# Optimization experiments

Hardware: AMD Instinct MI355X
Metric: run time of the kernel (lower is better)

## Reference

```python
import jax, jax.numpy as jnp
import numpy as np

B = 128      # graphs per batch
NPG = 40     # nodes per graph (<= MAXN)
N = B * NPG  # total nodes
E = 20000    # total edges
LP = 512     # protein sequence length
NPROT = 229  # KIBA proteins
MAXN = 45    # to_dense_batch max_num_nodes


def _gcn(x, W, b, src, dst, n):
    # PyG GCNConv: symmetric-normalized adjacency with self-loops.
    xw = x @ W
    deg = jnp.zeros((n,), xw.dtype).at[dst].add(1.0) + 1.0  # +1 for self-loop
    dinv = jax.lax.rsqrt(deg)
    msg = xw[src] * (dinv[src] * dinv[dst])[:, None]
    agg = jnp.zeros_like(xw).at[dst].add(msg) + xw * (1.0 / deg)[:, None]
    return agg + b


def _to_dense_batch(x, batch, num_graphs, max_nodes):
    n = x.shape[0]
    counts = jnp.zeros((num_graphs,), jnp.int32).at[batch].add(1)
    starts = jnp.concatenate([jnp.zeros((1,), jnp.int32), jnp.cumsum(counts)[:-1].astype(jnp.int32)])
    pos = jnp.arange(n, dtype=jnp.int32) - starts[batch]
    idx = batch * max_nodes + pos
    dense = jnp.zeros((num_graphs * max_nodes, x.shape[1]), x.dtype).at[idx].set(x)
    return dense.reshape(num_graphs, max_nodes, x.shape[1])


def setup_inputs() -> dict:
    key = jax.random.key(0)
    ks = jax.random.split(key, 32)
    xav = lambda k, s: jax.random.normal(k, s, jnp.float32) * jnp.sqrt(2.0 / (s[0] + s[-1]))
    x = jax.random.normal(ks[0], (N, 78), jnp.float32)
    src = jax.random.randint(ks[1], (E,), 0, N)
    dst = (src // NPG) * NPG + jax.random.randint(ks[2], (E,), 0, NPG)  # intra-graph edges
    edge_index = jnp.stack([src, dst]).astype(jnp.int32)
    target_id = jax.random.randint(ks[3], (B,), 0, NPROT).astype(jnp.int32)
    batch = (jnp.arange(N) // NPG).astype(jnp.int32)
    proteins = jax.random.normal(ks[4], (NPROT, LP, 1280), jnp.float32) * 0.1
    return dict(
        x=x, edge_index=edge_index, target_id=target_id, batch=batch, proteins=proteins,
        gW1=xav(ks[5], (78, 128)), gb1=jnp.zeros((128,), jnp.float32),
        gW2=xav(ks[6], (128, 128)), gb2=jnp.zeros((128,), jnp.float32),
        gW3=xav(ks[7], (128, 256)), gb3=jnp.zeros((256,), jnp.float32),
        fc1_W=xav(ks[8], (256, 1024)), fc1_b=jnp.zeros((1024,), jnp.float32),
        fc2_W=xav(ks[9], (1024, 128)), fc2_b=jnp.zeros((128,), jnp.float32),
        bert1_W=xav(ks[10], (1280, 128)), bert1_b=jnp.zeros((128,), jnp.float32),
        bert2_W=xav(ks[11], (128, 128)), bert2_b=jnp.zeros((128,), jnp.float32),
        W_b=xav(ks[12], (128, 128)), W_c=xav(ks[13], (32, 128)), W_p=xav(ks[14], (32, 128)),
        w_hc=xav(ks[15], (32, 1)), w_hp=xav(ks[16], (32, 1)),
        cat1_W=xav(ks[17], (256, 1024)), cat1_b=jnp.zeros((1024,), jnp.float32),
        cat2_W=xav(ks[18], (1024, 512)), cat2_b=jnp.zeros((512,), jnp.float32),
        out_W=xav(ks[19], (512, 1)), out_b=jnp.zeros((1,), jnp.float32),
    )


def _forward(x, proteins, gW1, gb1, gW2, gb2, gW3, gb3, fc1_W, fc1_b, fc2_W, fc2_b,
             bert1_W, bert1_b, bert2_W, bert2_b, W_b, W_c, W_p, w_hc, w_hp,
             cat1_W, cat1_b, cat2_W, cat2_b, out_W, out_b,
             edge_index, target_id, batch):
    relu, tanh = jax.nn.relu, jnp.tanh
    src, dst = edge_index[0], edge_index[1]
    # --- GCN stack (dropout is identity in eval) ---
    h = relu(_gcn(x, gW1, gb1, src, dst, x.shape[0]))
    h = relu(_gcn(h, gW2, gb2, src, dst, x.shape[0]))
    h = relu(_gcn(h, gW3, gb3, src, dst, x.shape[0]))  # [N, 256]
    hd = _to_dense_batch(h, batch, B, MAXN)            # [B, 45, 256]
    hd = relu(hd @ fc1_W + fc1_b)
    hd = relu(hd @ fc2_W + fc2_b)                      # [B, 45, 128]
    xc = jnp.transpose(hd, (0, 2, 1))                  # [B, 128, 45]
    # --- protein branch ---
    t = proteins[target_id]                            # [B, LP, 1280]
    t = relu(t @ bert1_W + bert1_b)
    t = relu(t @ bert2_W + bert2_b)                    # [B, LP, 128]
    # --- parallel co-attention ---
    C = tanh(jnp.einsum('blk,km,bms->bls', t, W_b, xc))       # [B, LP, 45]
    Wcx = jnp.einsum('km,bms->bks', W_c, xc)                  # [B, 32, 45]
    Wpt = jnp.einsum('km,blm->bkl', W_p, t)                   # [B, 32, LP]
    H_c = tanh(Wcx + jnp.einsum('bkl,bls->bks', Wpt, C))      # [B, 32, 45]
    H_p = tanh(Wpt + jnp.einsum('bks,bls->bkl', Wcx, C))      # [B, 32, LP]
    a_c = jax.nn.softmax(jnp.einsum('k,bks->bs', w_hc[:, 0], H_c), axis=-1)  # [B, 45]
    a_p = jax.nn.softmax(jnp.einsum('k,bkl->bl', w_hp[:, 0], H_p), axis=-1)  # [B, LP]
    c = jnp.einsum('bs,bms->bm', a_c, xc)                     # [B, 128]
    p = jnp.einsum('bl,blm->bm', a_p, t)                      # [B, 128]
    cp = jnp.concatenate([c, p], axis=1)                      # [B, 256]
    cp = relu(cp @ cat1_W + cat1_b)
    cp = relu(cp @ cat2_W + cat2_b)
    return cp @ out_W + out_b                                 # [B, 1]


def reference(x, edge_index, target_id, batch, proteins, gW1, gb1, gW2, gb2, gW3, gb3,
              fc1_W, fc1_b, fc2_W, fc2_b, bert1_W, bert1_b, bert2_W, bert2_b,
              W_b, W_c, W_p, w_hc, w_hp, cat1_W, cat1_b, cat2_W, cat2_b, out_W, out_b):
    return _forward(x, proteins, gW1, gb1, gW2, gb2, gW3, gb3, fc1_W, fc1_b, fc2_W, fc2_b,
                    bert1_W, bert1_b, bert2_W, bert2_b, W_b, W_c, W_p, w_hc, w_hp,
                    cat1_W, cat1_b, cat2_W, cat2_b, out_W, out_b,
                    edge_index, target_id, batch)
```

## Files before the change

### kernel.cpp

```cpp
#include <hip/hip_runtime.h>
#include <hip/hip_bf16.h>

typedef __hip_bfloat16 bf16;
typedef __bf16 bf16x8 __attribute__((ext_vector_type(8)));
typedef float f32x4 __attribute__((ext_vector_type(4)));

#define NB   128
#define NPGX 40
#define NNODE 5120
#define NE   20000
#define LPX  512
#define MAXNX 45

__device__ __forceinline__ void stv(float* p, float v) { *p = v; }
__device__ __forceinline__ void stv(bf16* p, float v) { *p = __float2bfloat16(v); }
__device__ __forceinline__ ushort f2bf(float f) {
    uint x = __float_as_uint(f);
    return (ushort)((x + 0x7fffu + ((x >> 16) & 1u)) >> 16);
}
__device__ __forceinline__ float bf2f(ushort u) { return __uint_as_float(((uint)u) << 16); }
__device__ __forceinline__ float dot4(f32x4 a, f32x4 b) {
    return a[0]*b[0] + a[1]*b[1] + a[2]*b[2] + a[3]*b[3];
}

template <typename TA, typename TO, int ACT, bool GATHER>
__global__ __launch_bounds__(256) void gemm_mfma(
    const TA* __restrict__ A, const ushort* __restrict__ BT, const float* __restrict__ bias,
    TO* __restrict__ C, int M, int N, int K, const int* __restrict__ tgt)
{
    __shared__ __align__(16) ushort sA[128][40];
    __shared__ __align__(16) ushort sB[128][40];
    const int t = threadIdx.x;
    const int lane = t & 63;
    const int wave = t >> 6;
    const int wr = wave >> 1, wc = wave & 1;
    const int m0 = blockIdx.x * 128;
    const int n0 = blockIdx.y * 128;
    const int fr = lane & 15;
    const int kh = lane >> 4;

    f32x4 acc[4][4] = {};

    for (int k0 = 0; k0 < K; k0 += 32) {
        if constexpr (sizeof(TA) == 2) {
            const ushort* Ap = (const ushort*)A;
#pragma unroll
            for (int i = 0; i < 2; i++) {
                int linear = i * 2048 + t * 8;
                int row = linear >> 5, k = linear & 31;
                long gr = m0 + row;
                uint4 v = *(const uint4*)(Ap + gr * (long)K + k0 + k);
                *(uint4*)&sA[row][k] = v;
            }
        } else {
            const float* Ap = (const float*)A;
#pragma unroll
            for (int i = 0; i < 4; i++) {
                int linear = i * 1024 + t * 4;
                int row = linear >> 5, k = linear & 31;
                long gr = m0 + row;
                if (GATHER) { int bb = (int)(gr >> 9); gr = (long)tgt[bb] * LPX + (gr & 511); }
                float4 v = *(const float4*)(Ap + gr * (long)K + k0 + k);
                ushort4 h;
                h.x = f2bf(v.x); h.y = f2bf(v.y); h.z = f2bf(v.z); h.w = f2bf(v.w);
                *(ushort4*)&sA[row][k] = h;
            }
        }
#pragma unroll
        for (int i = 0; i < 2; i++) {
            int linear = i * 2048 + t * 8;
            int row = linear >> 5, k = linear & 31;
            uint4 v = *(const uint4*)(BT + (long)(n0 + row) * K + k0 + k);
            *(uint4*)&sB[row][k] = v;
        }
        __syncthreads();

        bf16x8 a[4], b[4];
#pragma unroll
        for (int mf = 0; mf < 4; mf++)
            a[mf] = *(const bf16x8*)&sA[wr * 64 + mf * 16 + fr][kh * 8];
#pragma unroll
        for (int nf = 0; nf < 4; nf++)
            b[nf] = *(const bf16x8*)&sB[wc * 64 + nf * 16 + fr][kh * 8];
#pragma unroll
        for (int mf = 0; mf < 4; mf++)
#pragma unroll
            for (int nf = 0; nf < 4; nf++)
                acc[mf][nf] = __builtin_amdgcn_mfma_f32_16x16x32_bf16(a[mf], b[nf], acc[mf][nf], 0, 0, 0);
        __syncthreads();
    }

#pragma unroll
    for (int mf = 0; mf < 4; mf++) {
#pragma unroll
        for (int nf = 0; nf < 4; nf++) {
            int coln = n0 + wc * 64 + nf * 16 + fr;
            float bv = bias ? bias[coln] : 0.f;
#pragma unroll
            for (int r = 0; r < 4; r++) {
                int row = m0 + wr * 64 + mf * 16 + kh * 4 + r;
                float v = acc[mf][nf][r] + bv;
                if (ACT == 1) v = fmaxf(v, 0.f);
                else if (ACT == 2) v = tanhf(v);
                stv(&C[(long)row * N + coln], v);
            }
        }
    }
}

__global__ __launch_bounds__(256) void k_transp_all(
    const float* __restrict__ s0, const float* __restrict__ s1, const float* __restrict__ s2,
    const float* __restrict__ s3,
    ushort* __restrict__ d0, ushort* __restrict__ d1, ushort* __restrict__ d2,
    ushort* __restrict__ d3)
{
    __shared__ float s[32][33];
    int bid = blockIdx.x;
    const float* in; ushort* out; int K, N, b;
    if (bid < 256)      { in = s0; out = d0; K = 256;  N = 1024; b = bid; }
    else if (bid < 384) { in = s1; out = d1; K = 1024; N = 128;  b = bid - 256; }
    else if (bid < 544) { in = s2; out = d2; K = 1280; N = 128;  b = bid - 384; }
    else                { in = s3; out = d3; K = 128;  N = 128;  b = bid - 544; }
    int ktiles = K / 32;
    int kt = (b % ktiles) * 32, nt = (b / ktiles) * 32;
    int t = threadIdx.x;
    int tn = t & 31, tk = t >> 5;
#pragma unroll
    for (int i = 0; i < 4; i++)
        s[tk + i * 8][tn] = in[(long)(kt + tk + i * 8) * N + nt + tn];
    __syncthreads();
#pragma unroll
    for (int i = 0; i < 4; i++)
        out[(long)(nt + tk + i * 8) * K + kt + tn] = f2bf(s[tn][tk + i * 8]);
}

__global__ void k_count(const int* __restrict__ dst, int* __restrict__ cnt, int E) {
    int e = blockIdx.x * 256 + threadIdx.x;
    if (e < E) atomicAdd(&cnt[dst[e]], 1);
}

__global__ void k_scan(const int* __restrict__ cnt, int* __restrict__ row_start,
                       float* __restrict__ dinv, float* __restrict__ deginv, int n) {
    __shared__ int sd[1024];
    __shared__ int scarry;
    int t = threadIdx.x;
    if (t == 0) scarry = 0;
    __syncthreads();
    for (int base = 0; base < n; base += 1024) {
        int i = base + t;
        int v = (i < n) ? cnt[i] : 0;
        sd[t] = v;
        __syncthreads();
        for (int off = 1; off < 1024; off <<= 1) {
            int tmp = (t >= off) ? sd[t - off] : 0;
            __syncthreads();
            sd[t] += tmp;
            __syncthreads();
        }
        int carry = scarry;
        if (i < n) {
            row_start[i] = carry + sd[t] - v;
            float deg = (float)(v + 1);
            dinv[i] = rsqrtf(deg);
            deginv[i] = 1.f / deg;
        }
        __syncthreads();
        if (t == 1023) scarry = carry + sd[1023];
        __syncthreads();
    }
    if (t == 0) row_start[n] = scarry;
}

__global__ void k_fill(const int* __restrict__ src, const int* __restrict__ dst,
                       const int* __restrict__ row_start, int* __restrict__ cursor,
                       int* __restrict__ col, float* __restrict__ val,
                       const float* __restrict__ dinv, int E) {
    int e = blockIdx.x * 256 + threadIdx.x;
    if (e >= E) return;
    int d = dst[e], s = src[e];
    int p = atomicAdd(&cursor[d], 1);
    int idx = row_start[d] + p;
    col[idx] = s;
    val[idx] = dinv[s] * dinv[d];
}

__device__ __forceinline__ void gcn_gemm(const float (*hin)[132], float (*hout)[260],
                                         float (*sW)[260], const float* __restrict__ Wg,
                                         int K, int N, int NQ, int t) {
    f32x4 acc[10] = {};
    for (int k0 = 0; k0 < K; k0 += 32) {
        int kmax = min(32, K - k0);
        int kpad = (kmax + 3) & ~3;
        __syncthreads();
        for (int o = t; o < kpad * N; o += 256) {
            int row = o / N, c = o - row * N;
            sW[row][c] = (row < kmax) ? Wg[(k0 + row) * N + c] : 0.f;
        }
        __syncthreads();
        for (int kk = 0; kk < kpad; kk += 4) {
#pragma unroll 10
            for (int j = 0; j < NQ; j++) {
                int q = t + j * 256;
                int i = q / (N / 4), f = (q % (N / 4)) * 4;
                f32x4 hv = *(const f32x4*)&hin[i][k0 + kk];
#pragma unroll
                for (int d = 0; d < 4; d++) {
                    f32x4 wv = *(const f32x4*)&sW[kk + d][f];
                    acc[j][0] = fmaf(hv[d], wv[0], acc[j][0]);
                    acc[j][1] = fmaf(hv[d], wv[1], acc[j][1]);
                    acc[j][2] = fmaf(hv[d], wv[2], acc[j][2]);
                    acc[j][3] = fmaf(hv[d], wv[3], acc[j][3]);
                }
            }
        }
    }
    __syncthreads();
#pragma unroll 10
    for (int j = 0; j < NQ; j++) {
        int q = t + j * 256;
        int i = q / (N / 4), f = (q % (N / 4)) * 4;
        *(f32x4*)&hout[i][f] = acc[j];
    }
}

__device__ __forceinline__ void gcn_agg(const float (*hout)[260], float (*hin)[132],
                                        const float* __restrict__ bias,
                                        const float* __restrict__ deginv,
                                        const int* __restrict__ row_start,
                                        const int* __restrict__ col,
                                        const float* __restrict__ val,
                                        float* __restrict__ hd, int N, bool tohd, int g, int t) {
    int base = g * NPGX;
    for (int o = t; o < 40 * N; o += 256) {
        int i = o / N, f = o - i * N;
        float s = hout[i][f] * deginv[base + i];
        int e0 = row_start[base + i], e1 = row_start[base + i + 1];
        for (int e = e0; e < e1; e++) s += val[e] * hout[col[e] - base][f];
        s += bias[f];
        s = fmaxf(s, 0.f);
        if (tohd) hd[(g * MAXNX + i) * N + f] = s;
        else      hin[i][f] = s;
    }
    if (tohd) for (int o = t; o < 5 * N; o += 256) hd[(g * MAXNX + 40) * N + o] = 0.f;
}

__global__ __launch_bounds__(256) void k_gcn(
    const float* __restrict__ x,
    const float* __restrict__ W1, const float* __restrict__ b1,
    const float* __restrict__ W2, const float* __restrict__ b2,
    const float* __restrict__ W3, const float* __restrict__ b3,
    const float* __restrict__ deginv, const int* __restrict__ row_start,
    const int* __restrict__ col, const float* __restrict__ val,
    float* __restrict__ hd)
{
    int g = blockIdx.x, t = threadIdx.x;
    __shared__ __align__(16) float hin[40][132];
    __shared__ __align__(16) float hout[40][260];
    __shared__ __align__(16) float sW[32][260];
    for (int o = t; o < 40 * 78; o += 256) hin[o / 78][o % 78] = x[(g * NPGX + o / 78) * 78 + o % 78];
    for (int o = t; o < 80; o += 256) hin[o >> 1][78 + (o & 1)] = 0.f;
    gcn_gemm(hin, hout, sW, W1, 78, 128, 5, t);
    __syncthreads();
    gcn_agg(hout, hin, b1, deginv, row_start, col, val, nullptr, 128, false, g, t);
    __syncthreads();
    gcn_gemm(hin, hout, sW, W2, 128, 128, 5, t);
    __syncthreads();
    gcn_agg(hout, hin, b2, deginv, row_start, col, val, nullptr, 128, false, g, t);
    __syncthreads();
    gcn_gemm(hin, hout, sW, W3, 128, 256, 10, t);
    __syncthreads();
    gcn_agg(hout, nullptr, b3, deginv, row_start, col, val, hd, 256, true, g, t);
}

__global__ __launch_bounds__(512) void k_coatt(
    const ushort* __restrict__ t2, const float* __restrict__ hd2,
    const float* __restrict__ W_b, const float* __restrict__ W_c,
    const float* __restrict__ W_p, const float* __restrict__ w_hc,
    const float* __restrict__ w_hp, float* __restrict__ cp)
{
    __shared__ __align__(16) float  sx[48][132];
    __shared__ __align__(16) ushort sY[48][136];
    __shared__ __align__(16) ushort sWpb[32][136];
    __shared__ __align__(16) float  sWcx[32][48];
    __shared__ __align__(16) float  sHc[32][48];
    __shared__ __align__(16) ushort sT[128][136];
    __shared__ __align__(16) float  sC[128][52];
    __shared__ __align__(16) float  sWpt[32][132];
    __shared__ float  sLogit[512];
    __shared__ float  sLc[64];
    __shared__ float  swh[64];
    __shared__ float  sRed[8], sRed2[8];
    __shared__ float  sPc[4][128];

    const int b = blockIdx.x, tid = threadIdx.x;
    const int lane = tid & 63, wave = tid >> 6;
    const int fr = lane & 15, kh = lane >> 4;

    for (int o = tid; o < 48 * 32; o += 512) {
        int r = o >> 5, q = (o & 31) * 4;
        f32x4 v = {0.f, 0.f, 0.f, 0.f};
        if (r < 45) v = *(const f32x4*)&hd2[(b * 45 + r) * 128 + q];
        *(f32x4*)&sx[r][q] = v;
    }
    for (int o = tid; o < 32 * 32; o += 512) {
        int r = o >> 5, q = (o & 31) * 4;
        f32x4 v = *(const f32x4*)&W_p[r * 128 + q];
        sWpb[r][q] = f2bf(v[0]); sWpb[r][q + 1] = f2bf(v[1]);
        sWpb[r][q + 2] = f2bf(v[2]); sWpb[r][q + 3] = f2bf(v[3]);
    }
    if (tid < 64) swh[tid] = (tid < 32) ? w_hc[tid] : w_hp[tid - 32];
    for (int o = tid; o < 32 * 12; o += 512) {
        int r = o / 12, q = (o - r * 12) * 4;
        *(f32x4*)&sHc[r][q] = f32x4{0.f, 0.f, 0.f, 0.f};
    }
    __syncthreads();

    {
        int kg = tid >> 3, sg = tid & 7;
        float acc[12] = {};
        for (int m = 0; m < 128; m += 4) {
            f32x4 w0 = *(const f32x4*)&W_b[(2 * kg) * 128 + m];
            f32x4 w1 = *(const f32x4*)&W_b[(2 * kg + 1) * 128 + m];
#pragma unroll
            for (int u = 0; u < 6; u++) {
                f32x4 xv = *(const f32x4*)&sx[6 * sg + u][m];
                acc[u] += dot4(w0, xv);
                acc[6 + u] += dot4(w1, xv);
            }
        }
#pragma unroll
        for (int u = 0; u < 6; u++) {
            int s = 6 * sg + u;
            sY[s][2 * kg] = f2bf(acc[u]);
            sY[s][2 * kg + 1] = f2bf(acc[6 + u]);
        }
    }
    if (tid < 256) {
        int k = tid >> 3, sg = tid & 7;
        float acc[6] = {};
        for (int m = 0; m < 128; m += 4) {
            f32x4 w = *(const f32x4*)&W_c[k * 128 + m];
#pragma unroll
            for (int u = 0; u < 6; u++) {
                f32x4 xv = *(const f32x4*)&sx[6 * sg + u][m];
                acc[u] += dot4(w, xv);
            }
        }
#pragma unroll
        for (int u = 0; u < 6; u++) sWcx[k][6 * sg + u] = acc[u];
    }
    __syncthreads();

    const ushort* t2b = t2 + ((size_t)b * 512) * 128;

    for (int lc = 0; lc < 4; lc++) {
        {
            const ushort* srcp = t2b + lc * 128 * 128;
#pragma unroll
            for (int i = 0; i < 4; i++) {
                int idx = tid + i * 512;
                int row = idx >> 4, c8 = (idx & 15) * 8;
                *(uint4*)&sT[row][c8] = *(const uint4*)(srcp + row * 128 + c8);
            }
        }
        __syncthreads();
        {
            f32x4 cacc[3] = {};
            f32x4 wacc[2] = {};
#pragma unroll
            for (int ks = 0; ks < 4; ks++) {
                bf16x8 af = *(const bf16x8*)&sT[wave * 16 + fr][ks * 32 + kh * 8];
#pragma unroll
                for (int nt = 0; nt < 3; nt++) {
                    bf16x8 bf = *(const bf16x8*)&sY[nt * 16 + fr][ks * 32 + kh * 8];
                    cacc[nt] = __builtin_amdgcn_mfma_f32_16x16x32_bf16(af, bf, cacc[nt], 0, 0, 0);
                }
#pragma unroll
                for (int mt = 0; mt < 2; mt++) {
                    bf16x8 aw = *(const bf16x8*)&sWpb[mt * 16 + fr][ks * 32 + kh * 8];
                    wacc[mt] = __builtin_amdgcn_mfma_f32_16x16x32_bf16(aw, af, wacc[mt], 0, 0, 0);
                }
            }
#pragma unroll
            for (int nt = 0; nt < 3; nt++)
#pragma unroll
                for (int r = 0; r < 4; r++)
                    sC[wave * 16 + kh * 4 + r][nt * 16 + fr] = tanhf(cacc[nt][r]);
#pragma unroll
            for (int mt = 0; mt < 2; mt++)
#pragma unroll
                for (int r = 0; r < 4; r++)
                    sWpt[mt * 16 + kh * 4 + r][wave * 16 + fr] = wacc[mt][r];
        }
        __syncthreads();
        float hpacc[8];
        {
            if (tid < 384) {
                int k = tid / 12, sg = tid - (tid / 12) * 12;
                f32x4 a = {0.f, 0.f, 0.f, 0.f};
                for (int l = 0; l < 128; l++) {
                    float wv = sWpt[k][l];
                    f32x4 cv = *(const f32x4*)&sC[l][sg * 4];
                    a[0] = fmaf(wv, cv[0], a[0]); a[1] = fmaf(wv, cv[1], a[1]);
                    a[2] = fmaf(wv, cv[2], a[2]); a[3] = fmaf(wv, cv[3], a[3]);
                }
                f32x4 h = *(const f32x4*)&sHc[k][sg * 4];
                h[0] += a[0]; h[1] += a[1]; h[2] += a[2]; h[3] += a[3];
                *(f32x4*)&sHc[k][sg * 4] = h;
            }
            int kg = tid >> 5, li = tid & 31;
            float acc[8] = {};
            for (int s4 = 0; s4 < 48; s4 += 4) {
                f32x4 w0 = *(const f32x4*)&sWcx[2 * kg][s4];
                f32x4 w1 = *(const f32x4*)&sWcx[2 * kg + 1][s4];
#pragma unroll
                for (int u = 0; u < 4; u++) {
                    f32x4 cv = *(const f32x4*)&sC[li + 32 * u][s4];
                    acc[u] += dot4(w0, cv);
                    acc[4 + u] += dot4(w1, cv);
                }
            }
#pragma unroll
            for (int u = 0; u < 8; u++) hpacc[u] = acc[u];
        }
        __syncthreads();
        {
            int kg = tid >> 5, li = tid & 31;
#pragma unroll
            for (int u = 0; u < 4; u++) {
                sWpt[2 * kg][li + 32 * u] = tanhf(sWpt[2 * kg][li + 32 * u] + hpacc[u]);
                sWpt[2 * kg + 1][li + 32 * u] = tanhf(sWpt[2 * kg + 1][li + 32 * u] + hpacc[4 + u]);
            }
        }
        __syncthreads();
        if (tid < 128) {
            float a = 0.f;
            for (int k = 0; k < 32; k++) a += swh[32 + k] * sWpt[k][tid];
            sLogit[lc * 128 + tid] = a;
        }
        __syncthreads();
    }

    {
        int k = tid >> 4, si = tid & 15;
        if (tid < 512) {
            sHc[k][si] = tanhf(sWcx[k][si] + sHc[k][si]);
            sHc[k][si + 16] = tanhf(sWcx[k][si + 16] + sHc[k][si + 16]);
            sHc[k][si + 32] = tanhf(sWcx[k][si + 32] + sHc[k][si + 32]);
        }
    }
    __syncthreads();
    if (tid < 45) {
        float a = 0.f;
        for (int k = 0; k < 32; k++) a += swh[k] * sHc[k][tid];
        sLc[tid] = a;
    }
    __syncthreads();
    if (tid < 64) {
        float v = (tid < 45) ? sLc[tid] : -1e30f;
        float mx = v;
        for (int off = 32; off; off >>= 1) mx = fmaxf(mx, __shfl_xor(mx, off));
        float e = (tid < 45) ? expf(v - mx) : 0.f;
        float sm = e;
        for (int off = 32; off; off >>= 1) sm += __shfl_xor(sm, off);
        if (tid < 45) sLc[tid] = e / sm;
    }
    __syncthreads();
    if (tid < 128) {
        float c = 0.f;
        for (int s = 0; s < 45; s++) c += sLc[s] * sx[s][tid];
        cp[b * 256 + tid] = c;
    }
    {
        float v = sLogit[tid];
        float mx = v;
        for (int off = 32; off; off >>= 1) mx = fmaxf(mx, __shfl_xor(mx, off));
        if ((tid & 63) == 0) sRed[tid >> 6] = mx;
        __syncthreads();
        mx = sRed[0];
#pragma unroll
        for (int w = 1; w < 8; w++) mx = fmaxf(mx, sRed[w]);
        float e = expf(v - mx);
        float sm = e;
        for (int off = 32; off; off >>= 1) sm += __shfl_xor(sm, off);
        if ((tid & 63) == 0) sRed2[tid >> 6] = sm;
        __syncthreads();
        sm = 0.f;
#pragma unroll
        for (int w = 0; w < 8; w++) sm += sRed2[w];
        sLogit[tid] = e / sm;
    }
    __syncthreads();
    {
        int gq = tid >> 7, m = tid & 127;
        float pp = 0.f;
        for (int l = gq * 128; l < gq * 128 + 128; l++)
            pp += sLogit[l] * bf2f(t2b[l * 128 + m]);
        sPc[gq][m] = pp;
    }
    __syncthreads();
    if (tid < 128)
        cp[b * 256 + 128 + tid] = sPc[0][tid] + sPc[1][tid] + sPc[2][tid] + sPc[3][tid];
}

__global__ __launch_bounds__(256) void k_head(
    const float* __restrict__ cp, const float* __restrict__ W1, const float* __restrict__ b1,
    const float* __restrict__ W2, const float* __restrict__ b2,
    const float* __restrict__ outW, const float* __restrict__ outb, float* __restrict__ out)
{
    int b = blockIdx.x, t = threadIdx.x;
    __shared__ float sin[256];
    __shared__ float s1[1024];
    __shared__ float s2[512];
    __shared__ float r[4];
    sin[t] = cp[b * 256 + t];
    __syncthreads();
#pragma unroll
    for (int j = 0; j < 4; j++) {
        int n = t + j * 256;
        float a = b1[n];
        for (int k = 0; k < 256; k++) a += sin[k] * W1[k * 1024 + n];
        s1[n] = fmaxf(a, 0.f);
    }
    __syncthreads();
#pragma unroll
    for (int j = 0; j < 2; j++) {
        int n = t + j * 256;
        float a = b2[n];
        for (int k = 0; k < 1024; k++) a += s1[k] * W2[k * 512 + n];
        s2[n] = fmaxf(a, 0.f);
    }
    __syncthreads();
    float a = 0.f;
    for (int k = t; k < 512; k += 256) a += s2[k] * outW[k];
    for (int off = 32; off; off >>= 1) a += __shfl_xor(a, off);
    if ((t & 63) == 0) r[t >> 6] = a;
    __syncthreads();
    if (t == 0) out[b] = r[0] + r[1] + r[2] + r[3] + outb[0];
}

extern "C" void kernel_launch(void* const* d_in, const int* in_sizes, int n_in,
                              void* d_out, int out_size, void* d_ws, size_t ws_size,
                              hipStream_t stream) {
    const float* x        = (const float*)d_in[0];
    const int*   ei       = (const int*)d_in[1];
    const int*   tgt      = (const int*)d_in[2];
    const float* proteins = (const float*)d_in[4];
    const float* gW1 = (const float*)d_in[5];  const float* gb1 = (const float*)d_in[6];
    const float* gW2 = (const float*)d_in[7];  const float* gb2 = (const float*)d_in[8];
    const float* gW3 = (const float*)d_in[9];  const float* gb3 = (const float*)d_in[10];
    const float* fc1_W = (const float*)d_in[11]; const float* fc1_b = (const float*)d_in[12];
    const float* fc2_W = (const float*)d_in[13]; const float* fc2_b = (const float*)d_in[14];
    const float* bert1_W = (const float*)d_in[15]; const float* bert1_b = (const float*)d_in[16];
    const float* bert2_W = (const float*)d_in[17]; const float* bert2_b = (const float*)d_in[18];
    const float* W_b = (const float*)d_in[19];
    const float* W_c = (const float*)d_in[20];
    const float* W_p = (const float*)d_in[21];
    const float* w_hc = (const float*)d_in[22];
    const float* w_hp = (const float*)d_in[23];
    const float* cat1_W = (const float*)d_in[24]; const float* cat1_b = (const float*)d_in[25];
    const float* cat2_W = (const float*)d_in[26]; const float* cat2_b = (const float*)d_in[27];
    const float* out_W = (const float*)d_in[28]; const float* out_b = (const float*)d_in[29];

    const int* src = ei;
    const int* dst = ei + NE;

    char* w = (char*)d_ws;
    auto alloc = [&](size_t bytes) -> void* {
        void* p = (void*)w;
        w += (bytes + 255) & ~(size_t)255;
        return p;
    };
    int*   cnt       = (int*)alloc((size_t)2 * NNODE * 4);
    int*   cursor    = cnt + NNODE;
    int*   row_start = (int*)alloc((NNODE + 1) * 4);
    int*   colv      = (int*)alloc(NE * 4);
    float* valv      = (float*)alloc(NE * 4);
    float* dinv      = (float*)alloc(NNODE * 4);
    float* deginv    = (float*)alloc(NNODE * 4);
    float* hd        = (float*)alloc((size_t)5760 * 256 * 4);
    bf16*  fc1o      = (bf16*)alloc((size_t)5760 * 1024 * 2);
    float* hd2       = (float*)alloc((size_t)5760 * 128 * 4);
    bf16*  t1        = (bf16*)alloc((size_t)65536 * 128 * 2);
    bf16*  t2        = (bf16*)alloc((size_t)65536 * 128 * 2);
    float* cp        = (float*)alloc((size_t)NB * 256 * 4);
    ushort* fc1_WT   = (ushort*)alloc((size_t)1024 * 256 * 2);
    ushort* fc2_WT   = (ushort*)alloc((size_t)128 * 1024 * 2);
    ushort* bert1_WT = (ushort*)alloc((size_t)128 * 1280 * 2);
    ushort* bert2_WT = (ushort*)alloc((size_t)128 * 128 * 2);

    k_transp_all<<<560, 256, 0, stream>>>(fc1_W, fc2_W, bert1_W, bert2_W,
                                          fc1_WT, fc2_WT, bert1_WT, bert2_WT);
    hipMemsetAsync(cnt, 0, (size_t)2 * NNODE * 4, stream);
    k_count<<<(NE + 255) / 256, 256, 0, stream>>>(dst, cnt, NE);
    k_scan<<<1, 1024, 0, stream>>>(cnt, row_start, dinv, deginv, NNODE);
    k_fill<<<(NE + 255) / 256, 256, 0, stream>>>(src, dst, row_start, cursor, colv, valv, dinv, NE);
    k_gcn<<<NB, 256, 0, stream>>>(x, gW1, gb1, gW2, gb2, gW3, gb3,
                                  deginv, row_start, colv, valv, hd);
    gemm_mfma<float, bf16, 1, false><<<dim3(45, 8), 256, 0, stream>>>(hd, fc1_WT, fc1_b, fc1o, 5760, 1024, 256, nullptr);
    gemm_mfma<ushort, float, 1, false><<<dim3(45, 1), 256, 0, stream>>>((const ushort*)fc1o, fc2_WT, fc2_b, hd2, 5760, 128, 1024, nullptr);
    gemm_mfma<float, bf16, 1, true><<<dim3(512, 1), 256, 0, stream>>>(proteins, bert1_WT, bert1_b, t1, 65536, 128, 1280, tgt);
    gemm_mfma<ushort, bf16, 1, false><<<dim3(512, 1), 256, 0, stream>>>((const ushort*)t1, bert2_WT, bert2_b, t2, 65536, 128, 128, nullptr);
    k_coatt<<<NB, 512, 0, stream>>>((const ushort*)t2, hd2, W_b, W_c, W_p, w_hc, w_hp, cp);
    k_head<<<NB, 256, 0, stream>>>(cp, cat1_W, cat1_b, cat2_W, cat2_b, out_W, out_b, (float*)d_out);
}
```

Baseline: 1.240 ms.

## Fuse CSR build into GCN kernel, merge head into coattention, retile fc2 GEMM

Removes the separate count/scan/fill CSR kernels and memset by having each GCN block scan the edge list and build a per-graph CSR in shared memory, and folds the weight transpose into the same launch as extra blocks. The coattention kernel now also computes the MLP head, eliminating the cp buffer and one launch. The fc2 GEMM uses a new 64x64 tiled MFMA kernel to give more blocks. Risks include each graph block scanning all edges twice and a fixed EMAX edge cap per graph.

```diff
diff --git a/kernel.cpp b/kernel.cpp
--- a/kernel.cpp
+++ b/kernel.cpp
@@ -11,6 +11,7 @@
 #define NE   20000
 #define LPX  512
 #define MAXNX 45
+#define EMAX 512
 
 __device__ __forceinline__ void stv(float* p, float v) { *p = v; }
 __device__ __forceinline__ void stv(bf16* p, float v) { *p = __float2bfloat16(v); }
@@ -108,80 +109,59 @@
     }
 }
 
-__global__ __launch_bounds__(256) void k_transp_all(
-    const float* __restrict__ s0, const float* __restrict__ s1, const float* __restrict__ s2,
-    const float* __restrict__ s3,
-    ushort* __restrict__ d0, ushort* __restrict__ d1, ushort* __restrict__ d2,
-    ushort* __restrict__ d3)
+__global__ __launch_bounds__(256) void gemm_mfma64(
+    const ushort* __restrict__ A, const ushort* __restrict__ BT, const float* __restrict__ bias,
+    float* __restrict__ C, int M, int N, int K)
 {
-    __shared__ float s[32][33];
-    int bid = blockIdx.x;
-    const float* in; ushort* out; int K, N, b;
-    if (bid < 256)      { in = s0; out = d0; K = 256;  N = 1024; b = bid; }
-    else if (bid < 384) { in = s1; out = d1; K = 1024; N = 128;  b = bid - 256; }
-    else if (bid < 544) { in = s2; out = d2; K = 1280; N = 128;  b = bid - 384; }
-    else                { in = s3; out = d3; K = 128;  N = 128;  b = bid - 544; }
-    int ktiles = K / 32;
-    int kt = (b % ktiles) * 32, nt = (b / ktiles) * 32;
-    int t = threadIdx.x;
-    int tn = t & 31, tk = t >> 5;
-#pragma unroll
-    for (int i = 0; i < 4; i++)
-        s[tk + i * 8][tn] = in[(long)(kt + tk + i * 8) * N + nt + tn];
-    __syncthreads();
-#pragma unroll
-    for (int i = 0; i < 4; i++)
-        out[(long)(nt + tk + i * 8) * K + kt + tn] = f2bf(s[tn][tk + i * 8]);
-}
-
-__global__ void k_count(const int* __restrict__ dst, int* __restrict__ cnt, int E) {
-    int e = blockIdx.x * 256 + threadIdx.x;
-    if (e < E) atomicAdd(&cnt[dst[e]], 1);
-}
-
-__global__ void k_scan(const int* __restrict__ cnt, int* __restrict__ row_start,
-                       float* __restrict__ dinv, float* __restrict__ deginv, int n) {
-    __shared__ int sd[1024];
-    __shared__ int scarry;
-    int t = threadIdx.x;
-    if (t == 0) scarry = 0;
-    __syncthreads();
-    for (int base = 0; base < n; base += 1024) {
-        int i = base + t;
-        int v = (i < n) ? cnt[i] : 0;
-        sd[t] = v;
-        __syncthreads();
-        for (int off = 1; off < 1024; off <<= 1) {
-            int tmp = (t >= off) ? sd[t - off] : 0;
-            __syncthreads();
-            sd[t] += tmp;
-            __syncthreads();
-        }
-        int carry = scarry;
-        if (i < n) {
-            row_start[i] = carry + sd[t] - v;
-            float deg = (float)(v + 1);
-            dinv[i] = rsqrtf(deg);
-            deginv[i] = 1.f / deg;
-        }
-        __syncthreads();
-        if (t == 1023) scarry = carry + sd[1023];
-        __syncthreads();
-    }
-    if (t == 0) row_start[n] = scarry;
-}
-
-__global__ void k_fill(const int* __restrict__ src, const int* __restrict__ dst,
-                       const int* __restrict__ row_start, int* __restrict__ cursor,
-                       int* __restrict__ col, float* __restrict__ val,
-                       const float* __restrict__ dinv, int E) {
-    int e = blockIdx.x * 256 + threadIdx.x;
-    if (e >= E) return;
-    int d = dst[e], s = src[e];
-    int p = atomicAdd(&cursor[d], 1);
-    int idx = row_start[d] + p;
-    col[idx] = s;
-    val[idx] = dinv[s] * dinv[d];
+    __shared__ __align__(16) ushort sA[64][40];
+    __shared__ __align__(16) ushort sB[64][40];
+    const int t = threadIdx.x;
+    const int lane = t & 63;
+    const int wave = t >> 6;
+    const int wr = wave >> 1, wc = wave & 1;
+    const int m0 = blockIdx.x * 64;
+    const int n0 = blockIdx.y * 64;
+    const int fr = lane & 15;
+    const int kh = lane >> 4;
+
+    f32x4 acc[2][2] = {};
+
+    for (int k0 = 0; k0 < K; k0 += 32) {
+        {
+            int linear = t * 8;
+            int row = linear >> 5, k = linear & 31;
+            *(uint4*)&sA[row][k] = *(const uint4*)(A + (long)(m0 + row) * K + k0 + k);
+            *(uint4*)&sB[row][k] = *(const uint4*)(BT + (long)(n0 + row) * K + k0 + k);
+        }
+        __syncthreads();
+        bf16x8 a[2], b[2];
+#pragma unroll
+        for (int mf = 0; mf < 2; mf++)
+            a[mf] = *(const bf16x8*)&sA[wr * 32 + mf * 16 + fr][kh * 8];
+#pragma unroll
+        for (int nf = 0; nf < 2; nf++)
+            b[nf] = *(const bf16x8*)&sB[wc * 32 + nf * 16 + fr][kh * 8];
+#pragma unroll
+        for (int mf = 0; mf < 2; mf++)
+#pragma unroll
+            for (int nf = 0; nf < 2; nf++)
+                acc[mf][nf] = __builtin_amdgcn_mfma_f32_16x16x32_bf16(a[mf], b[nf], acc[mf][nf], 0, 0, 0);
+        __syncthreads();
+    }
+
+#pragma unroll
+    for (int mf = 0; mf < 2; mf++) {
+#pragma unroll
+        for (int nf = 0; nf < 2; nf++) {
+            int coln = n0 + wc * 32 + nf * 16 + fr;
+            float bv = bias[coln];
+#pragma unroll
+            for (int r = 0; r < 4; r++) {
+                int row = m0 + wr * 32 + mf * 16 + kh * 4 + r;
+                C[(long)row * N + coln] = fmaxf(acc[mf][nf][r] + bv, 0.f);
+            }
+        }
+    }
 }
 
 __device__ __forceinline__ void gcn_gemm(const float (*hin)[132], float (*hout)[260],
@@ -225,17 +205,16 @@
 
 __device__ __forceinline__ void gcn_agg(const float (*hout)[260], float (*hin)[132],
                                         const float* __restrict__ bias,
-                                        const float* __restrict__ deginv,
-                                        const int* __restrict__ row_start,
-                                        const int* __restrict__ col,
-                                        const float* __restrict__ val,
+                                        const float* __restrict__ dgi,
+                                        const int* __restrict__ rs,
+                                        const int* __restrict__ colv,
+                                        const float* __restrict__ valv,
                                         float* __restrict__ hd, int N, bool tohd, int g, int t) {
-    int base = g * NPGX;
     for (int o = t; o < 40 * N; o += 256) {
         int i = o / N, f = o - i * N;
-        float s = hout[i][f] * deginv[base + i];
-        int e0 = row_start[base + i], e1 = row_start[base + i + 1];
-        for (int e = e0; e < e1; e++) s += val[e] * hout[col[e] - base][f];
+        float s = hout[i][f] * dgi[i];
+        int e0 = rs[i], e1 = rs[i + 1];
+        for (int e = e0; e < e1; e++) s += valv[e] * hout[colv[e]][f];
         s += bias[f];
         s = fmaxf(s, 0.f);
         if (tohd) hd[(g * MAXNX + i) * N + f] = s;
@@ -244,39 +223,106 @@
     if (tohd) for (int o = t; o < 5 * N; o += 256) hd[(g * MAXNX + 40) * N + o] = 0.f;
 }
 
-__global__ __launch_bounds__(256) void k_gcn(
-    const float* __restrict__ x,
+__global__ __launch_bounds__(256) void k_prep(
+    const float* __restrict__ x, const int* __restrict__ ei,
     const float* __restrict__ W1, const float* __restrict__ b1,
     const float* __restrict__ W2, const float* __restrict__ b2,
     const float* __restrict__ W3, const float* __restrict__ b3,
-    const float* __restrict__ deginv, const int* __restrict__ row_start,
-    const int* __restrict__ col, const float* __restrict__ val,
-    float* __restrict__ hd)
+    float* __restrict__ hd,
+    const float* __restrict__ ws0, const float* __restrict__ ws1,
+    const float* __restrict__ ws2, const float* __restrict__ ws3,
+    ushort* __restrict__ wd0, ushort* __restrict__ wd1,
+    ushort* __restrict__ wd2, ushort* __restrict__ wd3)
 {
-    int g = blockIdx.x, t = threadIdx.x;
     __shared__ __align__(16) float hin[40][132];
     __shared__ __align__(16) float hout[40][260];
     __shared__ __align__(16) float sW[32][260];
-    for (int o = t; o < 40 * 78; o += 256) hin[o / 78][o % 78] = x[(g * NPGX + o / 78) * 78 + o % 78];
+    __shared__ int   s_cnt[40], s_cur[40], s_rs[41];
+    __shared__ int   s_col[EMAX];
+    __shared__ float s_val[EMAX];
+    __shared__ float s_dinv[40], s_dgi[40];
+
+    const int t = threadIdx.x;
+
+    if (blockIdx.x >= NB) {
+        float (*ts)[33] = reinterpret_cast<float(*)[33]>(&hin[0][0]);
+        int bid = blockIdx.x - NB;
+        const float* in; ushort* out; int K, N, b;
+        if (bid < 256)      { in = ws0; out = wd0; K = 256;  N = 1024; b = bid; }
+        else if (bid < 384) { in = ws1; out = wd1; K = 1024; N = 128;  b = bid - 256; }
+        else if (bid < 544) { in = ws2; out = wd2; K = 1280; N = 128;  b = bid - 384; }
+        else                { in = ws3; out = wd3; K = 128;  N = 128;  b = bid - 544; }
+        int ktiles = K / 32;
+        int kt = (b % ktiles) * 32, nt = (b / ktiles) * 32;
+        int tn = t & 31, tk = t >> 5;
+#pragma unroll
+        for (int i = 0; i < 4; i++)
+            ts[tk + i * 8][tn] = in[(long)(kt + tk + i * 8) * N + nt + tn];
+        __syncthreads();
+#pragma unroll
+        for (int i = 0; i < 4; i++)
+            out[(long)(nt + tk + i * 8) * K + kt + tn] = f2bf(ts[tn][tk + i * 8]);
+        return;
+    }
+
+    const int g = blockIdx.x;
+    const int base = g * NPGX;
+    const int* srcp = ei;
+    const int* dstp = ei + NE;
+
+    for (int o = t; o < 40; o += 256) { s_cnt[o] = 0; s_cur[o] = 0; }
+    for (int o = t; o < 40 * 78; o += 256) hin[o / 78][o % 78] = x[base * 78 + o];
     for (int o = t; o < 80; o += 256) hin[o >> 1][78 + (o & 1)] = 0.f;
+    __syncthreads();
+    for (int e = t; e < NE; e += 256) {
+        int dl = dstp[e] - base;
+        if ((unsigned)dl < 40u) atomicAdd(&s_cnt[dl], 1);
+    }
+    __syncthreads();
+    if (t == 0) {
+        int acc = 0;
+        for (int i = 0; i < 40; i++) { s_rs[i] = acc; acc += s_cnt[i]; }
+        s_rs[40] = acc;
+    }
+    if (t < 40) {
+        float deg = (float)(s_cnt[t] + 1);
+        s_dinv[t] = rsqrtf(deg);
+        s_dgi[t] = 1.f / deg;
+    }
+    __syncthreads();
+    for (int e = t; e < NE; e += 256) {
+        int dl = dstp[e] - base;
+        if ((unsigned)dl < 40u) {
+            int sl = srcp[e] - base;
+            int p = atomicAdd(&s_cur[dl], 1);
+            int idx = s_rs[dl] + p;
+            if (idx < EMAX) { s_col[idx] = sl; s_val[idx] = s_dinv[sl] * s_dinv[dl]; }
+        }
+    }
+    __syncthreads();
+
     gcn_gemm(hin, hout, sW, W1, 78, 128, 5, t);
     __syncthreads();
-    gcn_agg(hout, hin, b1, deginv, row_start, col, val, nullptr, 128, false, g, t);
+    gcn_agg(hout, hin, b1, s_dgi, s_rs, s_col, s_val, nullptr, 128, false, g, t);
     __syncthreads();
     gcn_gemm(hin, hout, sW, W2, 128, 128, 5, t);
     __syncthreads();
-    gcn_agg(hout, hin, b2, deginv, row_start, col, val, nullptr, 128, false, g, t);
+    gcn_agg(hout, hin, b2, s_dgi, s_rs, s_col, s_val, nullptr, 128, false, g, t);
     __syncthreads();
     gcn_gemm(hin, hout, sW, W3, 128, 256, 10, t);
     __syncthreads();
-    gcn_agg(hout, nullptr, b3, deginv, row_start, col, val, hd, 256, true, g, t);
-}
-
-__global__ __launch_bounds__(512) void k_coatt(
+    gcn_agg(hout, nullptr, b3, s_dgi, s_rs, s_col, s_val, hd, 256, true, g, t);
+}
+
+__global__ __launch_bounds__(512) void k_coatt_head(
     const ushort* __restrict__ t2, const float* __restrict__ hd2,
     const float* __restrict__ W_b, const float* __restrict__ W_c,
     const float* __restrict__ W_p, const float* __restrict__ w_hc,
-    const float* __restrict__ w_hp, float* __restrict__ cp)
+    const float* __restrict__ w_hp,
+    const float* __restrict__ cat1_W, const float* __restrict__ cat1_b,
+    const float* __restrict__ cat2_W, const float* __restrict__ cat2_b,
+    const float* __restrict__ outW, const float* __restrict__ outb,
+    float* __restrict__ out)
 {
     __shared__ __align__(16) float  sx[48][132];
     __shared__ __align__(16) ushort sY[48][136];
@@ -291,6 +337,7 @@
     __shared__ float  swh[64];
     __shared__ float  sRed[8], sRed2[8];
     __shared__ float  sPc[4][128];
+    __shared__ float  sCin[256];
 
     const int b = blockIdx.x, tid = threadIdx.x;
     const int lane = tid & 63, wave = tid >> 6;
@@ -443,11 +490,9 @@
 
     {
         int k = tid >> 4, si = tid & 15;
-        if (tid < 512) {
-            sHc[k][si] = tanhf(sWcx[k][si] + sHc[k][si]);
-            sHc[k][si + 16] = tanhf(sWcx[k][si + 16] + sHc[k][si + 16]);
-            sHc[k][si + 32] = tanhf(sWcx[k][si + 32] + sHc[k][si + 32]);
-        }
+        sHc[k][si] = tanhf(sWcx[k][si] + sHc[k][si]);
+        sHc[k][si + 16] = tanhf(sWcx[k][si + 16] + sHc[k][si + 16]);
+        sHc[k][si + 32] = tanhf(sWcx[k][si + 32] + sHc[k][si + 32]);
     }
     __syncthreads();
     if (tid < 45) {
@@ -469,7 +514,7 @@
     if (tid < 128) {
         float c = 0.f;
         for (int s = 0; s < 45; s++) c += sLc[s] * sx[s][tid];
-        cp[b * 256 + tid] = c;
+        sCin[tid] = c;
     }
     {
         float v = sLogit[tid];
@@ -500,43 +545,37 @@
     }
     __syncthreads();
     if (tid < 128)
-        cp[b * 256 + 128 + tid] = sPc[0][tid] + sPc[1][tid] + sPc[2][tid] + sPc[3][tid];
-}
-
-__global__ __launch_bounds__(256) void k_head(
-    const float* __restrict__ cp, const float* __restrict__ W1, const float* __restrict__ b1,
-    const float* __restrict__ W2, const float* __restrict__ b2,
-    const float* __restrict__ outW, const float* __restrict__ outb, float* __restrict__ out)
-{
-    int b = blockIdx.x, t = threadIdx.x;
-    __shared__ float sin[256];
-    __shared__ float s1[1024];
-    __shared__ float s2[512];
-    __shared__ float r[4];
-    sin[t] = cp[b * 256 + t];
-    __syncthreads();
-#pragma unroll
-    for (int j = 0; j < 4; j++) {
-        int n = t + j * 256;
-        float a = b1[n];
-        for (int k = 0; k < 256; k++) a += sin[k] * W1[k * 1024 + n];
-        s1[n] = fmaxf(a, 0.f);
-    }
-    __syncthreads();
+        sCin[128 + tid] = sPc[0][tid] + sPc[1][tid] + sPc[2][tid] + sPc[3][tid];
+    __syncthreads();
+
+    float* sH1 = (float*)&sT[0][0];
+    float* sH2 = sH1 + 1024;
 #pragma unroll
     for (int j = 0; j < 2; j++) {
-        int n = t + j * 256;
-        float a = b2[n];
-        for (int k = 0; k < 1024; k++) a += s1[k] * W2[k * 512 + n];
-        s2[n] = fmaxf(a, 0.f);
-    }
-    __syncthreads();
-    float a = 0.f;
-    for (int k = t; k < 512; k += 256) a += s2[k] * outW[k];
-    for (int off = 32; off; off >>= 1) a += __shfl_xor(a, off);
-    if ((t & 63) == 0) r[t >> 6] = a;
-    __syncthreads();
-    if (t == 0) out[b] = r[0] + r[1] + r[2] + r[3] + outb[0];
+        int n = tid + j * 512;
+        float a = cat1_b[n];
+        for (int k = 0; k < 256; k++) a = fmaf(sCin[k], cat1_W[k * 1024 + n], a);
+        sH1[n] = fmaxf(a, 0.f);
+    }
+    __syncthreads();
+    {
+        float a = cat2_b[tid];
+        for (int k = 0; k < 1024; k++) a = fmaf(sH1[k], cat2_W[k * 512 + tid], a);
+        sH2[tid] = fmaxf(a, 0.f);
+    }
+    __syncthreads();
+    {
+        float a = sH2[tid] * outW[tid];
+        for (int off = 32; off; off >>= 1) a += __shfl_xor(a, off);
+        if ((tid & 63) == 0) sRed[tid >> 6] = a;
+        __syncthreads();
+        if (tid == 0) {
+            float s = 0.f;
+#pragma unroll
+            for (int w = 0; w < 8; w++) s += sRed[w];
+            out[b] = s + outb[0];
+        }
+    }
 }
 
 extern "C" void kernel_launch(void* const* d_in, const int* in_sizes, int n_in,
@@ -562,45 +601,30 @@
     const float* cat2_W = (const float*)d_in[26]; const float* cat2_b = (const float*)d_in[27];
     const float* out_W = (const float*)d_in[28]; const float* out_b = (const float*)d_in[29];
 
-    const int* src = ei;
-    const int* dst = ei + NE;
-
     char* w = (char*)d_ws;
     auto alloc = [&](size_t bytes) -> void* {
         void* p = (void*)w;
         w += (bytes + 255) & ~(size_t)255;
         return p;
     };
-    int*   cnt       = (int*)alloc((size_t)2 * NNODE * 4);
-    int*   cursor    = cnt + NNODE;
-    int*   row_start = (int*)alloc((NNODE + 1) * 4);
-    int*   colv      = (int*)alloc(NE * 4);
-    float* valv      = (float*)alloc(NE * 4);
-    float* dinv      = (float*)alloc(NNODE * 4);
-    float* deginv    = (float*)alloc(NNODE * 4);
     float* hd        = (float*)alloc((size_t)5760 * 256 * 4);
     bf16*  fc1o      = (bf16*)alloc((size_t)5760 * 1024 * 2);
     float* hd2       = (float*)alloc((size_t)5760 * 128 * 4);
     bf16*  t1        = (bf16*)alloc((size_t)65536 * 128 * 2);
     bf16*  t2        = (bf16*)alloc((size_t)65536 * 128 * 2);
-    float* cp        = (float*)alloc((size_t)NB * 256 * 4);
     ushort* fc1_WT   = (ushort*)alloc((size_t)1024 * 256 * 2);
     ushort* fc2_WT   = (ushort*)alloc((size_t)128 * 1024 * 2);
     ushort* bert1_WT = (ushort*)alloc((size_t)128 * 1280 * 2);
     ushort* bert2_WT = (ushort*)alloc((size_t)128 * 128 * 2);
 
-    k_transp_all<<<560, 256, 0, stream>>>(fc1_W, fc2_W, bert1_W, bert2_W,
-                                          fc1_WT, fc2_WT, bert1_WT, bert2_WT);
-    hipMemsetAsync(cnt, 0, (size_t)2 * NNODE * 4, stream);
-    k_count<<<(NE + 255) / 256, 256, 0, stream>>>(dst, cnt, NE);
-    k_scan<<<1, 1024, 0, stream>>>(cnt, row_start, dinv, deginv, NNODE);
-    k_fill<<<(NE + 255) / 256, 256, 0, stream>>>(src, dst, row_start, cursor, colv, valv, dinv, NE);
-    k_gcn<<<NB, 256, 0, stream>>>(x, gW1, gb1, gW2, gb2, gW3, gb3,
-                                  deginv, row_start, colv, valv, hd);
+    k_prep<<<NB + 560, 256, 0, stream>>>(x, ei, gW1, gb1, gW2, gb2, gW3, gb3, hd,
+                                         fc1_W, fc2_W, bert1_W, bert2_W,
+                                         fc1_WT, fc2_WT, bert1_WT, bert2_WT);
     gemm_mfma<float, bf16, 1, false><<<dim3(45, 8), 256, 0, stream>>>(hd, fc1_WT, fc1_b, fc1o, 5760, 1024, 256, nullptr);
-    gemm_mfma<ushort, float, 1, false><<<dim3(45, 1), 256, 0, stream>>>((const ushort*)fc1o, fc2_WT, fc2_b, hd2, 5760, 128, 1024, nullptr);
+    gemm_mfma64<<<dim3(90, 2), 256, 0, stream>>>((const ushort*)fc1o, fc2_WT, fc2_b, hd2, 5760, 128, 1024);
     gemm_mfma<float, bf16, 1, true><<<dim3(512, 1), 256, 0, stream>>>(proteins, bert1_WT, bert1_b, t1, 65536, 128, 1280, tgt);
     gemm_mfma<ushort, bf16, 1, false><<<dim3(512, 1), 256, 0, stream>>>((const ushort*)t1, bert2_WT, bert2_b, t2, 65536, 128, 128, nullptr);
-    k_coatt<<<NB, 512, 0, stream>>>((const ushort*)t2, hd2, W_b, W_c, W_p, w_hc, w_hp, cp);
-    k_head<<<NB, 256, 0, stream>>>(cp, cat1_W, cat1_b, cat2_W, cat2_b, out_W, out_b, (float*)d_out);
-}
+    k_coatt_head<<<NB, 512, 0, stream>>>((const ushort*)t2, hd2, W_b, W_c, W_p, w_hc, w_hp,
+                                         cat1_W, cat1_b, cat2_W, cat2_b, out_W, out_b,
+                                         (float*)d_out);
+}
```

Result: faster. 1.165 ms (-6.1%).
